# Kernel optimization log

Hardware: AMD Instinct MI355X
Metric: run time of the kernel (lower is better)

Reference implementation:

```python
import jax, jax.numpy as jnp
import numpy as np

WINDOW_SIZE = 11
PAD = WINDOW_SIZE // 2
C1 = 0.01 ** 2
C2 = 0.03 ** 2


def _box_filter(x, window):
    # x: [B,1,H,W], window: [1,1,k,k] uniform kernel; SAME padding, depthwise (channel=1)
    return jax.lax.conv_general_dilated(
        x, window,
        window_strides=(1, 1),
        padding=[(PAD, PAD), (PAD, PAD)],
        dimension_numbers=('NCHW', 'OIHW', 'NCHW'),
        feature_group_count=1,
    )


def setup_inputs() -> dict:
    key = jax.random.key(0)
    k1, k2 = jax.random.split(key)
    B, C, H, W = 32, 1, 1024, 1024
    img1 = jax.random.uniform(k1, (B, C, H, W), dtype=jnp.float32)
    img2 = jax.random.uniform(k2, (B, C, H, W), dtype=jnp.float32)
    window = jnp.ones((1, 1, WINDOW_SIZE, WINDOW_SIZE), dtype=jnp.float32) / (WINDOW_SIZE * WINDOW_SIZE)
    return {"img1": img1, "img2": img2, "window": window}


def reference(img1, img2, window):
    mu1 = _box_filter(img1, window)
    mu2 = _box_filter(img2, window)
    mu1_sq = mu1 * mu1
    mu2_sq = mu2 * mu2
    mu1_mu2 = mu1 * mu2
    sigma1_sq = _box_filter(img1 * img1, window) - mu1_sq
    sigma2_sq = _box_filter(img2 * img2, window) - mu2_sq
    sigma12 = _box_filter(img1 * img2, window) - mu1_mu2
    ssim_map = ((2.0 * mu1_mu2 + C1) * (2.0 * sigma12 + C2)) / (
        (mu1_sq + mu2_sq + C1) * (sigma1_sq + sigma2_sq + C2)
    )
    # size_average=True -> scalar loss
    return 1.0 - jnp.mean(ssim_map)
```

## Files before the change

### kernel.cpp

```cpp
#include <hip/hip_runtime.h>

#define HH 1024
#define WW 1024
#define TW 116
#define WLP 128
#define NSLOT 1024
#define SSIM_C1 1e-4f
#define SSIM_C2 9e-4f

typedef float vf2 __attribute__((ext_vector_type(2)));
typedef __fp16 h2 __attribute__((ext_vector_type(2)));
typedef __fp16 h4 __attribute__((ext_vector_type(4)));

__global__ void ssim_ws_init(float* ws) { ws[threadIdx.x] = 0.f; }

__global__ __launch_bounds__(256, 4) void ssim_main(const float* __restrict__ img1,
                                                    const float* __restrict__ img2,
                                                    const float* __restrict__ window,
                                                    float* __restrict__ ws)
{
    __shared__ h4 cs4[4][8][WLP];

    const int tx = blockIdx.x;
    const int ty = blockIdx.y;
    const int b  = blockIdx.z;
    const int t  = threadIdx.x;
    const int q  = t >> 6;
    const int cg = t & 63;
    const int C0 = tx * TW;
    const int R0 = ty * 32 + q * 8;
    const size_t ibase = (size_t)b * (size_t)(HH * WW);
    const float w = window[0];

    {
        const int gc = C0 - 6 + 2 * cg;
        const int jb = __builtin_amdgcn_readfirstlane(R0 - 5);

        vf2 X[18], Y[18];
        const bool rin = (R0 >= 8) && (R0 <= HH - 16);
        const bool cin = (tx >= 1) && (tx <= 7);
        if (rin && cin) {
            const vf2* p1 = (const vf2*)(img1 + ibase + gc);
            const vf2* p2 = (const vf2*)(img2 + ibase + gc);
#pragma unroll
            for (int k = 0; k < 18; ++k) {
                const size_t off = (size_t)(jb + k) * (WW / 2);
                X[k] = p1[off];
                Y[k] = p2[off];
            }
        } else {
            const bool cok = (unsigned)gc < (unsigned)WW;
            const int gcc = min(max(gc, 0), WW - 2);
            const vf2* p1 = (const vf2*)(img1 + ibase + gcc);
            const vf2* p2 = (const vf2*)(img2 + ibase + gcc);
#pragma unroll
            for (int k = 0; k < 18; ++k) {
                const int j  = jb + k;
                const int jc = min(max(j, 0), HH - 1);
                const size_t off = (size_t)jc * (WW / 2);
                vf2 x = p1[off], y = p2[off];
                const bool ok = cok && ((unsigned)j < (unsigned)HH);
                if (!ok) { x = (vf2){0.f, 0.f}; y = (vf2){0.f, 0.f}; }
                X[k] = x; Y[k] = y;
            }
        }
        __builtin_amdgcn_sched_barrier(0);

        vf2 s1 = {0.f, 0.f}, s2 = {0.f, 0.f}, sp = {0.f, 0.f}, sq = {0.f, 0.f};
#pragma unroll
        for (int k = 0; k < 11; ++k) {
            const vf2 x = X[k], y = Y[k];
            const vf2 aa = x + y, dd = x - y;
            s1 += x; s2 += y;
            sp += aa * aa;
            sq += dd * dd;
        }
#pragma unroll
        for (int i = 0; i < 8; ++i) {
            if (i > 0) {
                const vf2 xn = X[10 + i], yn = Y[10 + i];
                const vf2 xo = X[i - 1],  yo = Y[i - 1];
                const vf2 an = xn + yn, dn = xn - yn;
                const vf2 ao = xo + yo, dq = xo - yo;
                s1 += xn - xo;
                s2 += yn - yo;
                sp += (an - ao) * (an + ao);
                sq += (dn - dq) * (dn + dq);
            }
            const h2 loa = __builtin_amdgcn_cvt_pkrtz(s1.x, s2.x);
            const h2 hia = __builtin_amdgcn_cvt_pkrtz(sp.x, sq.x);
            const h2 lob = __builtin_amdgcn_cvt_pkrtz(s1.y, s2.y);
            const h2 hib = __builtin_amdgcn_cvt_pkrtz(sp.y, sq.y);
            cs4[q][i][(2 * cg)     ^ i] = __builtin_shufflevector(loa, hia, 0, 1, 2, 3);
            cs4[q][i][(2 * cg + 1) ^ i] = __builtin_shufflevector(lob, hib, 0, 1, 2, 3);
        }
    }

    float ssum = 0.f;
    {
        const float u   = __builtin_amdgcn_rcpf(w);
        const float hu  = 0.5f  * u;
        const float qu  = 0.25f * u;
        const float C1p = SSIM_C1 * u * u;
        const float C2p = SSIM_C2 * u * u;
        const int r   = cg & 7;
        const int seg = cg >> 3;
        const int TWa = min(TW, WW - C0);
#pragma unroll 1
        for (int h = 0; h < 2; ++h) {
            const int c0 = seg * 16 + 8 * h;
            const int S  = min(8, TWa - c0);
            if (S > 0) {
                h4 v[19];
#pragma unroll
                for (int k = 0; k < 19; ++k) {
                    const int idx = (k >= 16) ? min(c0 + k, 127) : (c0 + k);
                    v[k] = cs4[q][r][idx ^ r];
                }
                __builtin_amdgcn_sched_barrier(0);

                h4 win = v[1] + v[2];
                win += v[3]; win += v[4]; win += v[5];
                win += v[6]; win += v[7]; win += v[8];
                win += v[9]; win += v[10];
#pragma unroll
                for (int p = 0; p < 8; ++p) {
                    if (p >= S) break;
                    win += v[p + 11];

                    const float S1 = (float)win.x, S2 = (float)win.y;
                    const float P  = (float)win.z, Q  = (float)win.w;
                    const float m11 = S1 * S1;
                    const float m22 = S2 * S2;
                    const float m12 = S1 * S2;
                    const float sigs = hu * (P + Q) - m11 - m22;
                    const float s12  = qu * (P - Q) - m12;
                    const float num  = (2.f * m12 + C1p) * (2.f * s12 + C2p);
                    const float den  = (m11 + m22 + C1p) * (sigs + C2p);
                    ssum += num * __builtin_amdgcn_rcpf(den);

                    win -= v[p + 1];
                }
            }
        }
    }

    float v = ssum;
#pragma unroll
    for (int off = 32; off > 0; off >>= 1) v += __shfl_down(v, off, 64);
    if (cg == 0) {
        const int bid  = tx + 9 * (ty + 32 * b);
        const int slot = (bid * 4 + q) & (NSLOT - 1);
        atomicAdd(ws + slot, v);
    }
}

__global__ void ssim_fin(const float* __restrict__ ws, float* __restrict__ out, int ntot) {
    const int lane = threadIdx.x;
    float v = 0.f;
#pragma unroll
    for (int k = 0; k < NSLOT / 64; ++k) v += ws[lane + 64 * k];
#pragma unroll
    for (int off = 32; off > 0; off >>= 1) v += __shfl_down(v, off, 64);
    if (lane == 0) out[0] = 1.f - v / (float)ntot;
}

extern "C" void kernel_launch(void* const* d_in, const int* in_sizes, int n_in,
                              void* d_out, int out_size, void* d_ws, size_t ws_size,
                              hipStream_t stream) {
    const float* img1 = (const float*)d_in[0];
    const float* img2 = (const float*)d_in[1];
    const float* win  = (const float*)d_in[2];
    float* out = (float*)d_out;
    float* ws  = (float*)d_ws;
    const int ntot = in_sizes[0];
    const int batches = ntot / (HH * WW);

    ssim_ws_init<<<dim3(1), dim3(NSLOT), 0, stream>>>(ws);
    dim3 grid((WW + TW - 1) / TW, HH / 32, batches);
    ssim_main<<<grid, dim3(256), 0, stream>>>(img1, img2, win, ws);
    ssim_fin<<<dim3(1), dim3(64), 0, stream>>>(ws, out, ntot);
}
```

Measured before the change: 73.61 us.

## Loop four row tiles per block and overlap global loads with previous tile's SSIM

Each block now processes four consecutive 32-row tiles in a loop, cutting the grid height by four. The global loads for the next tile are issued before the horizontal-window SSIM pass of the previous tile, so memory latency can overlap with compute. The second phase also handles 16 columns per lane in one pass, and the LDS row is padded to 144 entries. In exchange, register pressure rises (launch bounds drop to 3 waves), there are fewer blocks, and reusing the LDS buffer without barriers across tiles relies on each wave owning its own slice.

```diff
diff --git a/kernel.cpp b/kernel.cpp
--- a/kernel.cpp
+++ b/kernel.cpp
@@ -3,7 +3,7 @@
 #define HH 1024
 #define WW 1024
 #define TW 116
-#define WLP 128
+#define WLP 144
 #define NSLOT 1024
 #define SSIM_C1 1e-4f
 #define SSIM_C2 9e-4f
@@ -14,31 +14,82 @@
 
 __global__ void ssim_ws_init(float* ws) { ws[threadIdx.x] = 0.f; }
 
-__global__ __launch_bounds__(256, 4) void ssim_main(const float* __restrict__ img1,
+#define SSIM_EMIT do { \
+    const float S1 = (float)win.x, S2 = (float)win.y; \
+    const float P  = (float)win.z, Q  = (float)win.w; \
+    const float m11 = S1 * S1, m22 = S2 * S2, m12 = S1 * S2; \
+    const float sigs = hu * (P + Q) - m11 - m22; \
+    const float s12  = qu * (P - Q) - m12; \
+    const float num  = (2.f * m12 + C1p) * (2.f * s12 + C2p); \
+    const float den  = (m11 + m22 + C1p) * (sigs + C2p); \
+    ssum += num * __builtin_amdgcn_rcpf(den); \
+} while (0)
+
+#define PHASE2 do { if (S > 0) { \
+    h4 v[19]; \
+    _Pragma("unroll") \
+    for (int k = 0; k < 19; ++k) v[k] = cs4[q][r][(c0 + k) ^ r]; \
+    __builtin_amdgcn_sched_barrier(0); \
+    h4 win = v[1] + v[2]; \
+    win += v[3]; win += v[4]; win += v[5]; win += v[6]; \
+    win += v[7]; win += v[8]; win += v[9]; win += v[10]; \
+    _Pragma("unroll") \
+    for (int p = 0; p < 8; ++p) { \
+        if (p >= S) break; \
+        win += v[p + 11]; SSIM_EMIT; win -= v[p + 1]; \
+    } \
+    _Pragma("unroll") \
+    for (int k = 0; k < 8; ++k) v[k + 1] = cs4[q][r][(c0 + 19 + k) ^ r]; \
+    __builtin_amdgcn_sched_barrier(0); \
+    _Pragma("unroll") \
+    for (int p = 0; p < 8; ++p) { \
+        if (p + 8 >= S) break; \
+        win += v[p + 1]; SSIM_EMIT; win -= v[p + 9]; \
+    } \
+} } while (0)
+
+__global__ __launch_bounds__(256, 3) void ssim_main(const float* __restrict__ img1,
                                                     const float* __restrict__ img2,
                                                     const float* __restrict__ window,
                                                     float* __restrict__ ws)
 {
     __shared__ h4 cs4[4][8][WLP];
 
-    const int tx = blockIdx.x;
-    const int ty = blockIdx.y;
-    const int b  = blockIdx.z;
-    const int t  = threadIdx.x;
-    const int q  = t >> 6;
-    const int cg = t & 63;
-    const int C0 = tx * TW;
-    const int R0 = ty * 32 + q * 8;
+    const int tx  = blockIdx.x;
+    const int tyB = blockIdx.y;
+    const int b   = blockIdx.z;
+    const int t   = threadIdx.x;
+    const int q   = t >> 6;
+    const int cg  = t & 63;
+    const int C0  = tx * TW;
     const size_t ibase = (size_t)b * (size_t)(HH * WW);
     const float w = window[0];
 
-    {
-        const int gc = C0 - 6 + 2 * cg;
+    const int gc   = C0 - 6 + 2 * cg;
+    const bool cin = (tx >= 1) && (tx <= 7);
+    const bool cok = (unsigned)gc < (unsigned)WW;
+    const int gcc  = min(max(gc, 0), WW - 2);
+
+    const float u   = __builtin_amdgcn_rcpf(w);
+    const float hu  = 0.5f  * u;
+    const float qu  = 0.25f * u;
+    const float C1p = SSIM_C1 * u * u;
+    const float C2p = SSIM_C2 * u * u;
+    const int r   = cg & 7;
+    const int seg = cg >> 3;
+    const int c0  = seg * 16;
+    const int TWa = min(TW, WW - C0);
+    const int S   = min(16, TWa - c0);
+
+    float ssum = 0.f;
+    vf2 X[18], Y[18];
+
+#pragma unroll 1
+    for (int tt = 0; tt < 4; ++tt) {
+        const int R0 = tyB * 128 + tt * 32 + q * 8;
         const int jb = __builtin_amdgcn_readfirstlane(R0 - 5);
 
-        vf2 X[18], Y[18];
         const bool rin = (R0 >= 8) && (R0 <= HH - 16);
-        const bool cin = (tx >= 1) && (tx <= 7);
         if (rin && cin) {
             const vf2* p1 = (const vf2*)(img1 + ibase + gc);
             const vf2* p2 = (const vf2*)(img2 + ibase + gc);
@@ -49,8 +100,6 @@
                 Y[k] = p2[off];
             }
         } else {
-            const bool cok = (unsigned)gc < (unsigned)WW;
-            const int gcc = min(max(gc, 0), WW - 2);
             const vf2* p1 = (const vf2*)(img1 + ibase + gcc);
             const vf2* p2 = (const vf2*)(img2 + ibase + gcc);
 #pragma unroll
@@ -65,6 +114,10 @@
             }
         }
         __builtin_amdgcn_sched_barrier(0);
+
+        if (tt > 0) {
+            PHASE2;
+        }
 
         vf2 s1 = {0.f, 0.f}, s2 = {0.f, 0.f}, sp = {0.f, 0.f}, sq = {0.f, 0.f};
 #pragma unroll
@@ -96,62 +149,14 @@
         }
     }
 
-    float ssum = 0.f;
-    {
-        const float u   = __builtin_amdgcn_rcpf(w);
-        const float hu  = 0.5f  * u;
-        const float qu  = 0.25f * u;
-        const float C1p = SSIM_C1 * u * u;
-        const float C2p = SSIM_C2 * u * u;
-        const int r   = cg & 7;
-        const int seg = cg >> 3;
-        const int TWa = min(TW, WW - C0);
-#pragma unroll 1
-        for (int h = 0; h < 2; ++h) {
-            const int c0 = seg * 16 + 8 * h;
-            const int S  = min(8, TWa - c0);
-            if (S > 0) {
-                h4 v[19];
-#pragma unroll
-                for (int k = 0; k < 19; ++k) {
-                    const int idx = (k >= 16) ? min(c0 + k, 127) : (c0 + k);
-                    v[k] = cs4[q][r][idx ^ r];
-                }
-                __builtin_amdgcn_sched_barrier(0);
-
-                h4 win = v[1] + v[2];
-                win += v[3]; win += v[4]; win += v[5];
-                win += v[6]; win += v[7]; win += v[8];
-                win += v[9]; win += v[10];
-#pragma unroll
-                for (int p = 0; p < 8; ++p) {
-                    if (p >= S) break;
-                    win += v[p + 11];
-
-                    const float S1 = (float)win.x, S2 = (float)win.y;
-                    const float P  = (float)win.z, Q  = (float)win.w;
-                    const float m11 = S1 * S1;
-                    const float m22 = S2 * S2;
-                    const float m12 = S1 * S2;
-                    const float sigs = hu * (P + Q) - m11 - m22;
-                    const float s12  = qu * (P - Q) - m12;
-                    const float num  = (2.f * m12 + C1p) * (2.f * s12 + C2p);
-                    const float den  = (m11 + m22 + C1p) * (sigs + C2p);
-                    ssum += num * __builtin_amdgcn_rcpf(den);
-
-                    win -= v[p + 1];
-                }
-            }
-        }
-    }
+    PHASE2;
 
     float v = ssum;
 #pragma unroll
     for (int off = 32; off > 0; off >>= 1) v += __shfl_down(v, off, 64);
     if (cg == 0) {
-        const int bid  = tx + 9 * (ty + 32 * b);
-        const int slot = (bid * 4 + q) & (NSLOT - 1);
-        atomicAdd(ws + slot, v);
+        const int bid = tx + 9 * (tyB + 8 * b);
+        atomicAdd(ws + ((bid * 4 + q) & (NSLOT - 1)), v);
     }
 }
 
@@ -177,7 +182,7 @@
     const int batches = ntot / (HH * WW);
 
     ssim_ws_init<<<dim3(1), dim3(NSLOT), 0, stream>>>(ws);
-    dim3 grid((WW + TW - 1) / TW, HH / 32, batches);
+    dim3 grid((WW + TW - 1) / TW, HH / 128, batches);
     ssim_main<<<grid, dim3(256), 0, stream>>>(img1, img2, win, ws);
     ssim_fin<<<dim3(1), dim3(64), 0, stream>>>(ws, out, ntot);
 }
```

Measured after the change: 97.74 us. 1.33x slower.
